# Performance work log

Measured on AMD Instinct MI355X. Metric: run time of the kernel, lower is better.

The kernel has to match this reference:

```python
import jax, jax.numpy as jnp
import numpy as np

# All unordered pairs of 6 ligand sites (octahedral complex)
PAIRS = np.array([(i, j) for i in range(6) for j in range(i + 1, 6)], dtype=np.int32)  # [15, 2]

B, N_LIGS, D = 32768, 6, 64
IN_DIM = D + 2 * D  # core + lig_i + lig_j = 192
H1, H2 = 64, 32


def setup_inputs() -> dict:
    key = jax.random.key(0)
    ks = jax.random.split(key, 8)
    s = 0.05  # small init scale for numerical sanity
    return {
        "core": jax.random.normal(ks[0], (B, D), dtype=jnp.float32),
        "ligs": jax.random.normal(ks[1], (B, N_LIGS, D), dtype=jnp.float32),
        "W1": jax.random.normal(ks[2], (IN_DIM, H1), dtype=jnp.float32) * s,
        "b1": jnp.zeros((H1,), dtype=jnp.float32),
        "W2": jax.random.normal(ks[3], (H1, H2), dtype=jnp.float32) * s,
        "b2": jnp.zeros((H2,), dtype=jnp.float32),
        "W3": jax.random.normal(ks[4], (H2, 1), dtype=jnp.float32) * s,
        "b3": jnp.zeros((1,), dtype=jnp.float32),
    }


def _mlp(x, W1, b1, W2, b2, W3, b3):
    # Dense(softplus) -> Dense(softplus) -> Dense(1, linear); dropout is identity at inference
    h = jax.nn.softplus(x @ W1 + b1)
    h = jax.nn.softplus(h @ W2 + b2)
    return h @ W3 + b3  # [..., 1]


def reference(core, ligs, W1, b1, W2, b2, W3, b3):
    i_idx = jnp.asarray(PAIRS[:, 0])
    j_idx = jnp.asarray(PAIRS[:, 1])
    P = PAIRS.shape[0]
    li = ligs[:, i_idx, :]  # [B, P, D]
    lj = ligs[:, j_idx, :]  # [B, P, D]
    c = jnp.broadcast_to(core[:, None, :], (core.shape[0], P, core.shape[1]))
    x1 = jnp.concatenate([c, li, lj], axis=-1)  # [B, P, 3D]
    x2 = jnp.concatenate([c, lj, li], axis=-1)  # [B, P, 3D]
    res = 0.5 * (_mlp(x1, W1, b1, W2, b2, W3, b3) + _mlp(x2, W1, b1, W2, b2, W3, b3))  # [B, P, 1]
    return jnp.sum(res, axis=1)  # [B, 1]
```

## Files before the change

### kernel.cpp

```cpp
#include <hip/hip_runtime.h>
#include <hip/hip_fp16.h>
#include <stdint.h>


typedef __attribute__((ext_vector_type(8))) _Float16 f16x8;
typedef __attribute__((ext_vector_type(2))) __fp16   fp16v2;
typedef __attribute__((ext_vector_type(4))) float    f32x4;
typedef __attribute__((ext_vector_type(4))) unsigned int u32x4;

constexpr int   BPB       = 16;
constexpr int   NT        = 512;
constexpr int   T_STRIDE  = 1664;
constexpr int   Y_OFF     = BPB * T_STRIDE;
constexpr int   LDS_BYTES = Y_OFF + 128;

constexpr int   WS_W1F   = 0;
constexpr int   WS_W2T   = 24576;
constexpr int   WS_B1    = 28672;
constexpr int   WS_B2    = 28928;
constexpr int   WS_W3    = 29056;

constexpr float L2E = 1.4426950408889634f;
constexpr float LN2 = 0.6931471805599453f;

constexpr unsigned long long I_BITS =
  (0ull<<0)|(0ull<<3)|(0ull<<6)|(0ull<<9)|(0ull<<12)|
  (1ull<<15)|(1ull<<18)|(1ull<<21)|(1ull<<24)|
  (2ull<<27)|(2ull<<30)|(2ull<<33)|
  (3ull<<36)|(3ull<<39)|(4ull<<42);
constexpr unsigned long long J_BITS =
  (1ull<<0)|(2ull<<3)|(3ull<<6)|(4ull<<9)|(5ull<<12)|
  (2ull<<15)|(3ull<<18)|(4ull<<21)|(5ull<<24)|
  (3ull<<27)|(4ull<<30)|(5ull<<33)|
  (4ull<<36)|(5ull<<39)|(5ull<<42);

__device__ __forceinline__ float sp2(float s) {
  float t = __builtin_amdgcn_exp2f(s);
  return __builtin_amdgcn_logf(1.0f + t);
}

__device__ __forceinline__ __half2 h1pair(__half2 u, __half2 a, __half2 b,
                                          __half2 one2) {
  __half2 s = __hadd2(__hadd2(u, a), b);
  __half2 t = h2exp2(s);
  return h2log2(__hadd2(one2, t));
}

__global__ __launch_bounds__(256)
void prep(const float* __restrict__ W1, const float* __restrict__ b1,
          const float* __restrict__ W2, const float* __restrict__ b2,
          const float* __restrict__ W3, char* __restrict__ ws)
{
  const int t = (int)(blockIdx.x * blockDim.x + threadIdx.x);
  if (t < 12288) {
    const int e  = t & 7;
    const int ln = (t >> 3) & 15;
    const int qd = (t >> 7) & 3;
    const int ks = (t >> 9) & 1;
    const int nt = (t >> 10) & 3;
    const int sl = t >> 12;
    const int dg = sl * 64 + ks * 32 + qd * 8 + e;
    const int n  = nt * 16 + ln;
    ((uint16_t*)(ws + WS_W1F))[t] =
        __half_as_ushort(__float2half(W1[(size_t)dg * 64 + n] * L2E));
  } else if (t < 14336) {
    const int e = t - 12288;
    const int k = e >> 5, m = e & 31;
    *(uint16_t*)(ws + WS_W2T + (m * 64 + k) * 2) =
        __half_as_ushort(__float2half(W2[e]));
  } else if (t < 14400) {
    ((float*)(ws + WS_B1))[t - 14336] = b1[t - 14336] * L2E;
  } else if (t < 14432) {
    ((float*)(ws + WS_B2))[t - 14400] = b2[t - 14400] * L2E;
  } else if (t < 14464) {
    ((float*)(ws + WS_W3))[t - 14432] = W3[t - 14432] * LN2;
  }
}

__global__ __launch_bounds__(NT, 8)
void tb_fused(const float* __restrict__ core, const float* __restrict__ ligs,
              const char* __restrict__ ws,   const float* __restrict__ b3,
              float* __restrict__ out)
{
  extern __shared__ char smem[];
  const int tid  = (int)threadIdx.x;
  const int lane = tid & 63;
  const int ln   = lane & 15;
  const int qd   = lane >> 4;
  const int swz  = ln & 7;
  const int wv   = __builtin_amdgcn_readfirstlane(tid >> 6);
  const int b0   = (int)blockIdx.x * BPB;

  float* yred = (float*)(smem + Y_OFF);

  const int t1 = wv;
  const int t2 = wv + 8;
  const bool j2 = (wv < 5);

  float4 fA[2][4];
  {
    const int xr = (t1 == 0) ? 0 : (t1 <= 6 ? t1 : t1 - 6);
    const float* src = (xr == 0)
        ? (core + (size_t)(b0 + ln) * 64)
        : (ligs + ((size_t)(b0 + ln) * 6 + (size_t)(xr - 1)) * 64);
    #pragma unroll
    for (int ks = 0; ks < 2; ++ks) {
      fA[0][ks * 2 + 0] = *(const float4*)(src + ks * 32 + qd * 8);
      fA[0][ks * 2 + 1] = *(const float4*)(src + ks * 32 + qd * 8 + 4);
    }
  }
  if (j2) {
    const int xr = t2 - 6;
    const float* src = ligs + ((size_t)(b0 + ln) * 6 + (size_t)(xr - 1)) * 64;
    #pragma unroll
    for (int ks = 0; ks < 2; ++ks) {
      fA[1][ks * 2 + 0] = *(const float4*)(src + ks * 32 + qd * 8);
      fA[1][ks * 2 + 1] = *(const float4*)(src + ks * 32 + qd * 8 + 4);
    }
  }
  if (tid < BPB) yred[tid] = 0.0f;

  union AFr { f16x8 v; fp16v2 p[4]; } Xf[2][2];
  #pragma unroll
  for (int jj = 0; jj < 2; ++jj) {
    if (jj == 1 && !j2) break;
    #pragma unroll
    for (int ks = 0; ks < 2; ++ks) {
      Xf[jj][ks].p[0] = __builtin_amdgcn_cvt_pkrtz(fA[jj][ks*2].x, fA[jj][ks*2].y);
      Xf[jj][ks].p[1] = __builtin_amdgcn_cvt_pkrtz(fA[jj][ks*2].z, fA[jj][ks*2].w);
      Xf[jj][ks].p[2] = __builtin_amdgcn_cvt_pkrtz(fA[jj][ks*2+1].x, fA[jj][ks*2+1].y);
      Xf[jj][ks].p[3] = __builtin_amdgcn_cvt_pkrtz(fA[jj][ks*2+1].z, fA[jj][ks*2+1].w);
    }
  }

  #pragma unroll
  for (int jj = 0; jj < 2; ++jj) {
    if (jj == 1 && !j2) break;
    const int t  = (jj == 0) ? t1 : t2;
    const int sl = (t == 0) ? 0 : (t <= 6 ? 1 : 2);
    #pragma unroll
    for (int nt = 0; nt < 4; ++nt) {
      f32x4 c;
      if (t == 0) {
        c = *(const f32x4*)(ws + WS_B1 + (nt * 16 + qd * 4) * 4);
      } else {
        c = (f32x4){0.f, 0.f, 0.f, 0.f};
      }
      #pragma unroll
      for (int ks = 0; ks < 2; ++ks) {
        const f16x8 Wf = *(const f16x8*)(ws + WS_W1F
            + (size_t)(sl * 4096 + nt * 1024 + ks * 512 + qd * 128 + ln * 8) * 2);
        c = __builtin_amdgcn_mfma_f32_16x16x32_f16(Wf, Xf[jj][ks].v, c, 0, 0, 0);
      }
      union PK { uint2 u; __half2 h[2]; } pk;
      pk.h[0] = __halves2half2(__float2half(c[0]), __float2half(c[1]));
      pk.h[1] = __halves2half2(__float2half(c[2]), __float2half(c[3]));
      *(uint2*)(smem + (size_t)ln * T_STRIDE + t * 128
                + ((((nt << 1) + (qd >> 1)) ^ swz) << 4) + (qd & 1) * 8) = pk.u;
    }
  }

  f16x8 W2f[2][2];
  #pragma unroll
  for (int nt = 0; nt < 2; ++nt)
    #pragma unroll
    for (int ks = 0; ks < 2; ++ks)
      W2f[nt][ks] = *(const f16x8*)(ws + WS_W2T
          + ((nt * 16 + ln) * 64 + ks * 32 + qd * 8) * 2);
  float b2v[2], w3v[2];
  #pragma unroll
  for (int nt = 0; nt < 2; ++nt) {
    b2v[nt] = ((const float*)(ws + WS_B2))[nt * 16 + ln];
    w3v[nt] = ((const float*)(ws + WS_W3))[nt * 16 + ln];
  }

  __syncthreads();

  const int qr = wv;
  const __half2 one2 = __float2half2_rn(1.0f);
  const char* Tb = smem + (size_t)ln * T_STRIDE;
  const int k0 = ((qd)     ^ swz) << 4;
  const int k1 = ((qd + 4) ^ swz) << 4;

  union U4 { u32x4 u; __half2 h[4]; };

  U4 du0, du1;
  du0.u = *(const u32x4*)(Tb + k0);
  du1.u = *(const u32x4*)(Tb + k1);

  float yacc[4] = {0.f, 0.f, 0.f, 0.f};

  #pragma unroll 2
  for (int t3 = 0; t3 < 4; ++t3) {
    const int q = qr + 8 * t3;
    if (q >= 30) break;
    const int p  = q >> 1;
    const int iv = (int)((I_BITS >> (3 * p)) & 7ull);
    const int jv = (int)((J_BITS >> (3 * p)) & 7ull);
    const int An = (q & 1) ? jv : iv;
    const int Bn = (q & 1) ? iv : jv;
    const char* TA = Tb + (1 + An) * 128;
    const char* TB = Tb + (7 + Bn) * 128;

    U4 da0, db0, da1, db1;
    da0.u = *(const u32x4*)(TA + k0);
    db0.u = *(const u32x4*)(TB + k0);
    da1.u = *(const u32x4*)(TA + k1);
    db1.u = *(const u32x4*)(TB + k1);

    union { f16x8 v; __half2 h[4]; } A0, A1;
    #pragma unroll
    for (int w = 0; w < 4; ++w) A0.h[w] = h1pair(du0.h[w], da0.h[w], db0.h[w], one2);
    #pragma unroll
    for (int w = 0; w < 4; ++w) A1.h[w] = h1pair(du1.h[w], da1.h[w], db1.h[w], one2);

    f32x4 c0 = {b2v[0], b2v[0], b2v[0], b2v[0]};
    f32x4 c1 = {b2v[1], b2v[1], b2v[1], b2v[1]};
    c0 = __builtin_amdgcn_mfma_f32_16x16x32_f16(A0.v, W2f[0][0], c0, 0, 0, 0);
    c0 = __builtin_amdgcn_mfma_f32_16x16x32_f16(A1.v, W2f[0][1], c0, 0, 0, 0);
    c1 = __builtin_amdgcn_mfma_f32_16x16x32_f16(A0.v, W2f[1][0], c1, 0, 0, 0);
    c1 = __builtin_amdgcn_mfma_f32_16x16x32_f16(A1.v, W2f[1][1], c1, 0, 0, 0);

    #pragma unroll
    for (int reg = 0; reg < 4; ++reg) {
      yacc[reg] += sp2(c0[reg]) * w3v[0] + sp2(c1[reg]) * w3v[1];
    }
  }

  #pragma unroll
  for (int reg = 0; reg < 4; ++reg) {
    float v = yacc[reg];
    v += __shfl_xor(v, 1);
    v += __shfl_xor(v, 2);
    v += __shfl_xor(v, 4);
    v += __shfl_xor(v, 8);
    yacc[reg] = v;
  }
  if (ln == 0) {
    #pragma unroll
    for (int reg = 0; reg < 4; ++reg)
      atomicAdd(&yred[qd * 4 + reg], yacc[reg]);
  }
  __syncthreads();
  if (tid < BPB) out[b0 + tid] = 0.5f * yred[tid] + 15.0f * b3[0];
}

extern "C" void kernel_launch(void* const* d_in, const int* in_sizes, int n_in,
                              void* d_out, int out_size, void* d_ws, size_t ws_size,
                              hipStream_t stream) {
  const float* core = (const float*)d_in[0];
  const float* ligs = (const float*)d_in[1];
  const float* W1   = (const float*)d_in[2];
  const float* b1   = (const float*)d_in[3];
  const float* W2   = (const float*)d_in[4];
  const float* b2   = (const float*)d_in[5];
  const float* W3   = (const float*)d_in[6];
  const float* b3   = (const float*)d_in[7];
  float* out = (float*)d_out;
  char*  ws  = (char*)d_ws;

  const int B = in_sizes[0] / 64;
  const int grid = B / BPB;

  prep<<<dim3(57), dim3(256), 0, stream>>>(W1, b1, W2, b2, W3, ws);

  (void)hipFuncSetAttribute((const void*)tb_fused,
                            hipFuncAttributeMaxDynamicSharedMemorySize, LDS_BYTES);
  tb_fused<<<dim3(grid), dim3(NT), LDS_BYTES, stream>>>(
      core, ligs, ws, b3, out);
}
```

Baseline: 128.0 us.

## Process four 16-row tiles per block with double-buffered layer-1 pipeline

Each block now handles four 16-row tiles with 1024 threads. Thirteen waves load and run layer 1 for the next tile into a second LDS buffer while all sixteen waves run layer 2 on the current tile. The LDS atomic reduction is replaced by per-wave partial buffers that a single wave sums, and weights are loaded once per block instead of once per tile. The cost is fewer blocks, so less grid parallelism, and a 1024-thread block with about 55KB of LDS, which limits occupancy. The launch bound of 8 is likely not reachable at this block size and may push register limits.

```diff
diff --git a/kernel.cpp b/kernel.cpp
--- a/kernel.cpp
+++ b/kernel.cpp
@@ -8,11 +8,13 @@
 typedef __attribute__((ext_vector_type(4))) float    f32x4;
 typedef __attribute__((ext_vector_type(4))) unsigned int u32x4;
 
-constexpr int   BPB       = 16;
-constexpr int   NT        = 512;
+constexpr int   BPT       = 16;
+constexpr int   NTILES    = 4;
+constexpr int   NT        = 1024;
 constexpr int   T_STRIDE  = 1664;
-constexpr int   Y_OFF     = BPB * T_STRIDE;
-constexpr int   LDS_BYTES = Y_OFF + 128;
+constexpr int   TBUF      = BPT * T_STRIDE;
+constexpr int   PB_OFF    = 2 * TBUF;
+constexpr int   LDS_BYTES = PB_OFF + 2048;
 
 constexpr int   WS_W1F   = 0;
 constexpr int   WS_W2T   = 24576;
@@ -77,6 +79,41 @@
   }
 }
 
+#define P2_UNIT(Q_)                                                          \
+  {                                                                          \
+    const int p_  = (Q_) >> 1;                                               \
+    const int iv_ = (int)((I_BITS >> (3 * p_)) & 7ull);                      \
+    const int jv_ = (int)((J_BITS >> (3 * p_)) & 7ull);                      \
+    const int An_ = ((Q_) & 1) ? jv_ : iv_;                                  \
+    const int Bn_ = ((Q_) & 1) ? iv_ : jv_;                                  \
+    const char* TA_ = Tb + (1 + An_) * 128;                                  \
+    const char* TB_ = Tb + (7 + Bn_) * 128;                                  \
+    U4 da0_, db0_, da1_, db1_;                                               \
+    da0_.u = *(const u32x4*)(TA_ + k0);                                      \
+    db0_.u = *(const u32x4*)(TB_ + k0);                                      \
+    da1_.u = *(const u32x4*)(TA_ + k1);                                      \
+    db1_.u = *(const u32x4*)(TB_ + k1);                                      \
+    union AH_ { f16x8 v; __half2 h[4]; } A0_, A1_;                           \
+    A0_.h[0] = h1pair(du0.h[0], da0_.h[0], db0_.h[0], one2);                 \
+    A0_.h[1] = h1pair(du0.h[1], da0_.h[1], db0_.h[1], one2);                 \
+    A0_.h[2] = h1pair(du0.h[2], da0_.h[2], db0_.h[2], one2);                 \
+    A0_.h[3] = h1pair(du0.h[3], da0_.h[3], db0_.h[3], one2);                 \
+    A1_.h[0] = h1pair(du1.h[0], da1_.h[0], db1_.h[0], one2);                 \
+    A1_.h[1] = h1pair(du1.h[1], da1_.h[1], db1_.h[1], one2);                 \
+    A1_.h[2] = h1pair(du1.h[2], da1_.h[2], db1_.h[2], one2);                 \
+    A1_.h[3] = h1pair(du1.h[3], da1_.h[3], db1_.h[3], one2);                 \
+    f32x4 c0_ = {b2v0, b2v0, b2v0, b2v0};                                    \
+    f32x4 c1_ = {b2v1, b2v1, b2v1, b2v1};                                    \
+    c0_ = __builtin_amdgcn_mfma_f32_16x16x32_f16(A0_.v, W2f[0][0], c0_, 0, 0, 0); \
+    c0_ = __builtin_amdgcn_mfma_f32_16x16x32_f16(A1_.v, W2f[0][1], c0_, 0, 0, 0); \
+    c1_ = __builtin_amdgcn_mfma_f32_16x16x32_f16(A0_.v, W2f[1][0], c1_, 0, 0, 0); \
+    c1_ = __builtin_amdgcn_mfma_f32_16x16x32_f16(A1_.v, W2f[1][1], c1_, 0, 0, 0); \
+    yacc0 += sp2(c0_[0]) * w3v0 + sp2(c1_[0]) * w3v1;                        \
+    yacc1 += sp2(c0_[1]) * w3v0 + sp2(c1_[1]) * w3v1;                        \
+    yacc2 += sp2(c0_[2]) * w3v0 + sp2(c1_[2]) * w3v1;                        \
+    yacc3 += sp2(c0_[3]) * w3v0 + sp2(c1_[3]) * w3v1;                        \
+  }
+
 __global__ __launch_bounds__(NT, 8)
 void tb_fused(const float* __restrict__ core, const float* __restrict__ ligs,
               const char* __restrict__ ws,   const float* __restrict__ b3,
@@ -89,76 +126,19 @@
   const int qd   = lane >> 4;
   const int swz  = ln & 7;
   const int wv   = __builtin_amdgcn_readfirstlane(tid >> 6);
-  const int b0   = (int)blockIdx.x * BPB;
-
-  float* yred = (float*)(smem + Y_OFF);
-
-  const int t1 = wv;
-  const int t2 = wv + 8;
-  const bool j2 = (wv < 5);
-
-  float4 fA[2][4];
-  {
-    const int xr = (t1 == 0) ? 0 : (t1 <= 6 ? t1 : t1 - 6);
-    const float* src = (xr == 0)
-        ? (core + (size_t)(b0 + ln) * 64)
-        : (ligs + ((size_t)(b0 + ln) * 6 + (size_t)(xr - 1)) * 64);
-    #pragma unroll
-    for (int ks = 0; ks < 2; ++ks) {
-      fA[0][ks * 2 + 0] = *(const float4*)(src + ks * 32 + qd * 8);
-      fA[0][ks * 2 + 1] = *(const float4*)(src + ks * 32 + qd * 8 + 4);
-    }
-  }
-  if (j2) {
-    const int xr = t2 - 6;
-    const float* src = ligs + ((size_t)(b0 + ln) * 6 + (size_t)(xr - 1)) * 64;
-    #pragma unroll
-    for (int ks = 0; ks < 2; ++ks) {
-      fA[1][ks * 2 + 0] = *(const float4*)(src + ks * 32 + qd * 8);
-      fA[1][ks * 2 + 1] = *(const float4*)(src + ks * 32 + qd * 8 + 4);
-    }
-  }
-  if (tid < BPB) yred[tid] = 0.0f;
-
-  union AFr { f16x8 v; fp16v2 p[4]; } Xf[2][2];
-  #pragma unroll
-  for (int jj = 0; jj < 2; ++jj) {
-    if (jj == 1 && !j2) break;
-    #pragma unroll
-    for (int ks = 0; ks < 2; ++ks) {
-      Xf[jj][ks].p[0] = __builtin_amdgcn_cvt_pkrtz(fA[jj][ks*2].x, fA[jj][ks*2].y);
-      Xf[jj][ks].p[1] = __builtin_amdgcn_cvt_pkrtz(fA[jj][ks*2].z, fA[jj][ks*2].w);
-      Xf[jj][ks].p[2] = __builtin_amdgcn_cvt_pkrtz(fA[jj][ks*2+1].x, fA[jj][ks*2+1].y);
-      Xf[jj][ks].p[3] = __builtin_amdgcn_cvt_pkrtz(fA[jj][ks*2+1].z, fA[jj][ks*2+1].w);
-    }
-  }
-
-  #pragma unroll
-  for (int jj = 0; jj < 2; ++jj) {
-    if (jj == 1 && !j2) break;
-    const int t  = (jj == 0) ? t1 : t2;
-    const int sl = (t == 0) ? 0 : (t <= 6 ? 1 : 2);
-    #pragma unroll
-    for (int nt = 0; nt < 4; ++nt) {
-      f32x4 c;
-      if (t == 0) {
-        c = *(const f32x4*)(ws + WS_B1 + (nt * 16 + qd * 4) * 4);
-      } else {
-        c = (f32x4){0.f, 0.f, 0.f, 0.f};
-      }
-      #pragma unroll
-      for (int ks = 0; ks < 2; ++ks) {
-        const f16x8 Wf = *(const f16x8*)(ws + WS_W1F
-            + (size_t)(sl * 4096 + nt * 1024 + ks * 512 + qd * 128 + ln * 8) * 2);
-        c = __builtin_amdgcn_mfma_f32_16x16x32_f16(Wf, Xf[jj][ks].v, c, 0, 0, 0);
-      }
-      union PK { uint2 u; __half2 h[2]; } pk;
-      pk.h[0] = __halves2half2(__float2half(c[0]), __float2half(c[1]));
-      pk.h[1] = __halves2half2(__float2half(c[2]), __float2half(c[3]));
-      *(uint2*)(smem + (size_t)ln * T_STRIDE + t * 128
-                + ((((nt << 1) + (qd >> 1)) ^ swz) << 4) + (qd & 1) * 8) = pk.u;
-    }
-  }
+  const int b0   = (int)blockIdx.x * (BPT * NTILES);
+
+  const int k0 = ((qd)     ^ swz) << 4;
+  const int k1 = ((qd + 4) ^ swz) << 4;
+  const __half2 one2 = __float2half2_rn(1.0f);
+  union U4 { u32x4 u; __half2 h[4]; };
+
+  const float b3v = b3[0];
+
+  const bool haveJob = (wv >= 3);
+  const int  jt      = wv - 3;
+  const int  jsl     = (jt == 0) ? 0 : (jt <= 6 ? 1 : 2);
+  const int  jlig    = (jt <= 6) ? (jt - 1) : (jt - 7);
 
   f16x8 W2f[2][2];
   #pragma unroll
@@ -167,82 +147,137 @@
     for (int ks = 0; ks < 2; ++ks)
       W2f[nt][ks] = *(const f16x8*)(ws + WS_W2T
           + ((nt * 16 + ln) * 64 + ks * 32 + qd * 8) * 2);
-  float b2v[2], w3v[2];
+  const float b2v0 = ((const float*)(ws + WS_B2))[ln];
+  const float b2v1 = ((const float*)(ws + WS_B2))[16 + ln];
+  const float w3v0 = ((const float*)(ws + WS_W3))[ln];
+  const float w3v1 = ((const float*)(ws + WS_W3))[16 + ln];
+
+  {
+    float4 fA[4];
+    if (haveJob) {
+      const int bb = b0 + ln;
+      const float* src = (jt == 0)
+          ? (core + (size_t)bb * 64)
+          : (ligs + ((size_t)bb * 6 + (size_t)jlig) * 64);
+      #pragma unroll
+      for (int ks = 0; ks < 2; ++ks) {
+        fA[ks * 2 + 0] = *(const float4*)(src + ks * 32 + qd * 8);
+        fA[ks * 2 + 1] = *(const float4*)(src + ks * 32 + qd * 8 + 4);
+      }
+      union AFr { f16x8 v; fp16v2 p[4]; } Xf[2];
+      #pragma unroll
+      for (int ks = 0; ks < 2; ++ks) {
+        Xf[ks].p[0] = __builtin_amdgcn_cvt_pkrtz(fA[ks*2].x, fA[ks*2].y);
+        Xf[ks].p[1] = __builtin_amdgcn_cvt_pkrtz(fA[ks*2].z, fA[ks*2].w);
+        Xf[ks].p[2] = __builtin_amdgcn_cvt_pkrtz(fA[ks*2+1].x, fA[ks*2+1].y);
+        Xf[ks].p[3] = __builtin_amdgcn_cvt_pkrtz(fA[ks*2+1].z, fA[ks*2+1].w);
+      }
+      char* Tn = smem + (size_t)ln * T_STRIDE;
+      #pragma unroll
+      for (int nt = 0; nt < 4; ++nt) {
+        f32x4 c;
+        if (jt == 0) c = *(const f32x4*)(ws + WS_B1 + (nt * 16 + qd * 4) * 4);
+        else         c = (f32x4){0.f, 0.f, 0.f, 0.f};
+        #pragma unroll
+        for (int ks = 0; ks < 2; ++ks) {
+          const f16x8 Wf = *(const f16x8*)(ws + WS_W1F
+              + (size_t)(jsl * 4096 + nt * 1024 + ks * 512 + qd * 128 + ln * 8) * 2);
+          c = __builtin_amdgcn_mfma_f32_16x16x32_f16(Wf, Xf[ks].v, c, 0, 0, 0);
+        }
+        union PK { uint2 u; __half2 h[2]; } pk;
+        pk.h[0] = __halves2half2(__float2half(c[0]), __float2half(c[1]));
+        pk.h[1] = __halves2half2(__float2half(c[2]), __float2half(c[3]));
+        *(uint2*)(Tn + jt * 128
+                  + ((((nt << 1) + (qd >> 1)) ^ swz) << 4) + (qd & 1) * 8) = pk.u;
+      }
+    }
+  }
+  __syncthreads();
+
   #pragma unroll
-  for (int nt = 0; nt < 2; ++nt) {
-    b2v[nt] = ((const float*)(ws + WS_B2))[nt * 16 + ln];
-    w3v[nt] = ((const float*)(ws + WS_W3))[nt * 16 + ln];
-  }
-
-  __syncthreads();
-
-  const int qr = wv;
-  const __half2 one2 = __float2half2_rn(1.0f);
-  const char* Tb = smem + (size_t)ln * T_STRIDE;
-  const int k0 = ((qd)     ^ swz) << 4;
-  const int k1 = ((qd + 4) ^ swz) << 4;
-
-  union U4 { u32x4 u; __half2 h[4]; };
-
-  U4 du0, du1;
-  du0.u = *(const u32x4*)(Tb + k0);
-  du1.u = *(const u32x4*)(Tb + k1);
-
-  float yacc[4] = {0.f, 0.f, 0.f, 0.f};
-
-  #pragma unroll 2
-  for (int t3 = 0; t3 < 4; ++t3) {
-    const int q = qr + 8 * t3;
-    if (q >= 30) break;
-    const int p  = q >> 1;
-    const int iv = (int)((I_BITS >> (3 * p)) & 7ull);
-    const int jv = (int)((J_BITS >> (3 * p)) & 7ull);
-    const int An = (q & 1) ? jv : iv;
-    const int Bn = (q & 1) ? iv : jv;
-    const char* TA = Tb + (1 + An) * 128;
-    const char* TB = Tb + (7 + Bn) * 128;
-
-    U4 da0, db0, da1, db1;
-    da0.u = *(const u32x4*)(TA + k0);
-    db0.u = *(const u32x4*)(TB + k0);
-    da1.u = *(const u32x4*)(TA + k1);
-    db1.u = *(const u32x4*)(TB + k1);
-
-    union { f16x8 v; __half2 h[4]; } A0, A1;
+  for (int k = 0; k < NTILES; ++k) {
+    const char* Tb = smem + (size_t)(k & 1) * TBUF + (size_t)ln * T_STRIDE;
+
+    if (k > 0 && wv == 2 && lane < 16) {
+      const float* pp = (const float*)(smem + PB_OFF + ((k - 1) & 1) * 1024);
+      float s = 0.f;
+      #pragma unroll
+      for (int w = 0; w < 16; ++w) s += pp[w * 16 + lane];
+      out[b0 + (k - 1) * 16 + lane] = 0.5f * s + 15.0f * b3v;
+    }
+
+    float4 fA[4];
+    if (k < NTILES - 1 && haveJob) {
+      const int bb = b0 + (k + 1) * 16 + ln;
+      const float* src = (jt == 0)
+          ? (core + (size_t)bb * 64)
+          : (ligs + ((size_t)bb * 6 + (size_t)jlig) * 64);
+      #pragma unroll
+      for (int ks = 0; ks < 2; ++ks) {
+        fA[ks * 2 + 0] = *(const float4*)(src + ks * 32 + qd * 8);
+        fA[ks * 2 + 1] = *(const float4*)(src + ks * 32 + qd * 8 + 4);
+      }
+    }
+
+    U4 du0, du1;
+    du0.u = *(const u32x4*)(Tb + k0);
+    du1.u = *(const u32x4*)(Tb + k1);
+    float yacc0 = 0.f, yacc1 = 0.f, yacc2 = 0.f, yacc3 = 0.f;
+    P2_UNIT(wv)
+    if (wv < 14) { P2_UNIT(wv + 16) }
+
+    yacc0 += __shfl_xor(yacc0, 1); yacc1 += __shfl_xor(yacc1, 1);
+    yacc2 += __shfl_xor(yacc2, 1); yacc3 += __shfl_xor(yacc3, 1);
+    yacc0 += __shfl_xor(yacc0, 2); yacc1 += __shfl_xor(yacc1, 2);
+    yacc2 += __shfl_xor(yacc2, 2); yacc3 += __shfl_xor(yacc3, 2);
+    yacc0 += __shfl_xor(yacc0, 4); yacc1 += __shfl_xor(yacc1, 4);
+    yacc2 += __shfl_xor(yacc2, 4); yacc3 += __shfl_xor(yacc3, 4);
+    yacc0 += __shfl_xor(yacc0, 8); yacc1 += __shfl_xor(yacc1, 8);
+    yacc2 += __shfl_xor(yacc2, 8); yacc3 += __shfl_xor(yacc3, 8);
+    if (ln == 0) {
+      float* pb = (float*)(smem + PB_OFF + (k & 1) * 1024);
+      *(f32x4*)(pb + wv * 16 + qd * 4) = (f32x4){yacc0, yacc1, yacc2, yacc3};
+    }
+
+    if (k < NTILES - 1 && haveJob) {
+      union AFr { f16x8 v; fp16v2 p[4]; } Xf[2];
+      #pragma unroll
+      for (int ks = 0; ks < 2; ++ks) {
+        Xf[ks].p[0] = __builtin_amdgcn_cvt_pkrtz(fA[ks*2].x, fA[ks*2].y);
+        Xf[ks].p[1] = __builtin_amdgcn_cvt_pkrtz(fA[ks*2].z, fA[ks*2].w);
+        Xf[ks].p[2] = __builtin_amdgcn_cvt_pkrtz(fA[ks*2+1].x, fA[ks*2+1].y);
+        Xf[ks].p[3] = __builtin_amdgcn_cvt_pkrtz(fA[ks*2+1].z, fA[ks*2+1].w);
+      }
+      char* Tn = smem + (size_t)((k + 1) & 1) * TBUF + (size_t)ln * T_STRIDE;
+      #pragma unroll
+      for (int nt = 0; nt < 4; ++nt) {
+        f32x4 c;
+        if (jt == 0) c = *(const f32x4*)(ws + WS_B1 + (nt * 16 + qd * 4) * 4);
+        else         c = (f32x4){0.f, 0.f, 0.f, 0.f};
+        #pragma unroll
+        for (int ks = 0; ks < 2; ++ks) {
+          const f16x8 Wf = *(const f16x8*)(ws + WS_W1F
+              + (size_t)(jsl * 4096 + nt * 1024 + ks * 512 + qd * 128 + ln * 8) * 2);
+          c = __builtin_amdgcn_mfma_f32_16x16x32_f16(Wf, Xf[ks].v, c, 0, 0, 0);
+        }
+        union PK { uint2 u; __half2 h[2]; } pk;
+        pk.h[0] = __halves2half2(__float2half(c[0]), __float2half(c[1]));
+        pk.h[1] = __halves2half2(__float2half(c[2]), __float2half(c[3]));
+        *(uint2*)(Tn + jt * 128
+                  + ((((nt << 1) + (qd >> 1)) ^ swz) << 4) + (qd & 1) * 8) = pk.u;
+      }
+    }
+
+    __syncthreads();
+  }
+
+  if (wv == 2 && lane < 16) {
+    const float* pp = (const float*)(smem + PB_OFF + ((NTILES - 1) & 1) * 1024);
+    float s = 0.f;
     #pragma unroll
-    for (int w = 0; w < 4; ++w) A0.h[w] = h1pair(du0.h[w], da0.h[w], db0.h[w], one2);
-    #pragma unroll
-    for (int w = 0; w < 4; ++w) A1.h[w] = h1pair(du1.h[w], da1.h[w], db1.h[w], one2);
-
-    f32x4 c0 = {b2v[0], b2v[0], b2v[0], b2v[0]};
-    f32x4 c1 = {b2v[1], b2v[1], b2v[1], b2v[1]};
-    c0 = __builtin_amdgcn_mfma_f32_16x16x32_f16(A0.v, W2f[0][0], c0, 0, 0, 0);
-    c0 = __builtin_amdgcn_mfma_f32_16x16x32_f16(A1.v, W2f[0][1], c0, 0, 0, 0);
-    c1 = __builtin_amdgcn_mfma_f32_16x16x32_f16(A0.v, W2f[1][0], c1, 0, 0, 0);
-    c1 = __builtin_amdgcn_mfma_f32_16x16x32_f16(A1.v, W2f[1][1], c1, 0, 0, 0);
-
-    #pragma unroll
-    for (int reg = 0; reg < 4; ++reg) {
-      yacc[reg] += sp2(c0[reg]) * w3v[0] + sp2(c1[reg]) * w3v[1];
-    }
-  }
-
-  #pragma unroll
-  for (int reg = 0; reg < 4; ++reg) {
-    float v = yacc[reg];
-    v += __shfl_xor(v, 1);
-    v += __shfl_xor(v, 2);
-    v += __shfl_xor(v, 4);
-    v += __shfl_xor(v, 8);
-    yacc[reg] = v;
-  }
-  if (ln == 0) {
-    #pragma unroll
-    for (int reg = 0; reg < 4; ++reg)
-      atomicAdd(&yred[qd * 4 + reg], yacc[reg]);
-  }
-  __syncthreads();
-  if (tid < BPB) out[b0 + tid] = 0.5f * yred[tid] + 15.0f * b3[0];
+    for (int w = 0; w < 16; ++w) s += pp[w * 16 + lane];
+    out[b0 + (NTILES - 1) * 16 + lane] = 0.5f * s + 15.0f * b3v;
+  }
 }
 
 extern "C" void kernel_launch(void* const* d_in, const int* in_sizes, int n_in,
@@ -260,7 +295,7 @@
   char*  ws  = (char*)d_ws;
 
   const int B = in_sizes[0] / 64;
-  const int grid = B / BPB;
+  const int grid = B / (BPT * NTILES);
 
   prep<<<dim3(57), dim3(256), 0, stream>>>(W1, b1, W2, b2, W3, ws);
 
```

After: 215.5 us. 1.68x slower.
